# Optimization experiments

Hardware: AMD Instinct MI355X
Metric: run time of the kernel (lower is better)

Reference implementation:

```python
import jax, jax.numpy as jnp
import numpy as np

DIM = 512
HEADS = 8
HEAD_DIM = DIM // HEADS
SCALE = HEAD_DIM ** -0.5
EPS = 1e-5


def setup_inputs() -> dict:
    key = jax.random.key(0)
    ks = jax.random.split(key, 6)
    B, N, C = 4, 2048, DIM
    x = jax.random.normal(ks[0], (B, N, C), dtype=jnp.float32)
    w_qkv = jax.random.normal(ks[1], (C, 3 * C), dtype=jnp.float32) * (C ** -0.5)
    w_proj = jax.random.normal(ks[2], (C, C), dtype=jnp.float32) * (C ** -0.5)
    b_proj = jax.random.normal(ks[3], (C,), dtype=jnp.float32) * 0.02
    gamma = jnp.ones((C,), dtype=jnp.float32)
    beta = jnp.zeros((C,), dtype=jnp.float32)
    return {"x": x, "w_qkv": w_qkv, "w_proj": w_proj, "b_proj": b_proj,
            "gamma": gamma, "beta": beta}


def reference(x, w_qkv, w_proj, b_proj, gamma, beta):
    B, N, C = x.shape
    # LayerNorm over channel dim
    mu = jnp.mean(x, axis=-1, keepdims=True)
    var = jnp.mean(jnp.square(x - mu), axis=-1, keepdims=True)
    xn = (x - mu) * jax.lax.rsqrt(var + EPS) * gamma + beta
    # QKV projection (fp32, no bias)
    qkv = xn @ w_qkv  # [B, N, 3C]
    qkv = qkv.reshape(B, N, 3, HEADS, HEAD_DIM)
    q = jnp.transpose(qkv[:, :, 0], (0, 2, 1, 3))  # [B, H, N, D]
    k = jnp.transpose(qkv[:, :, 1], (0, 2, 1, 3))
    v = jnp.transpose(qkv[:, :, 2], (0, 2, 1, 3))
    attn = jnp.einsum('bhnd,bhmd->bhnm', q, k) * SCALE
    attn = jax.nn.softmax(attn, axis=-1)
    out = jnp.einsum('bhnm,bhmd->bhnd', attn, v)  # [B, H, N, D]
    out = jnp.transpose(out, (0, 2, 1, 3)).reshape(B, N, C)
    out = out @ w_proj + b_proj
    return x + out
```

## Files before the change

### kernel.cpp

```cpp
#include <hip/hip_runtime.h>
#include <hip/hip_bf16.h>
#include <math.h>

typedef _Float16 f16;
typedef _Float16 half8 __attribute__((ext_vector_type(8)));
typedef _Float16 half4 __attribute__((ext_vector_type(4)));
typedef float f32x4 __attribute__((ext_vector_type(4)));

#define DIMC 512
#define HEADS 8
#define HD 64
#define BB 4
#define NN 2048
#define MM (BB*NN)
#define NQKV (3*DIMC)
#define SCALE 0.125f
#define LOG2E 1.44269504f
#define EPSLN 1e-5f

__device__ __forceinline__ void g2l16(const void* g, void* l) {
    __builtin_amdgcn_global_load_lds(
        (const __attribute__((address_space(1))) unsigned int*)g,
        (__attribute__((address_space(3))) unsigned int*)l, 16, 0, 0);
}

__device__ __forceinline__ void ln_rows(const float* __restrict__ x,
                                        const float* __restrict__ gamma,
                                        const float* __restrict__ beta,
                                        f16* __restrict__ xn, int blk) {
    int w = threadIdx.x >> 6;
    int lane = threadIdx.x & 63;
    int row = blk * 4 + w;
    const float* xr = x + (size_t)row * DIMC;
    float4 v0 = ((const float4*)xr)[lane * 2];
    float4 v1 = ((const float4*)xr)[lane * 2 + 1];
    float s = v0.x + v0.y + v0.z + v0.w + v1.x + v1.y + v1.z + v1.w;
#pragma unroll
    for (int off = 1; off < 64; off <<= 1) s += __shfl_xor(s, off);
    float mu = s * (1.0f / DIMC);
    float d0 = v0.x - mu, d1 = v0.y - mu, d2 = v0.z - mu, d3 = v0.w - mu;
    float d4 = v1.x - mu, d5 = v1.y - mu, d6 = v1.z - mu, d7 = v1.w - mu;
    float s2 = d0*d0 + d1*d1 + d2*d2 + d3*d3 + d4*d4 + d5*d5 + d6*d6 + d7*d7;
#pragma unroll
    for (int off = 1; off < 64; off <<= 1) s2 += __shfl_xor(s2, off);
    float rstd = rsqrtf(s2 * (1.0f / DIMC) + EPSLN);
    float4 g0 = ((const float4*)gamma)[lane * 2];
    float4 g1 = ((const float4*)gamma)[lane * 2 + 1];
    float4 b0 = ((const float4*)beta)[lane * 2];
    float4 b1 = ((const float4*)beta)[lane * 2 + 1];
    half8 o;
    o[0] = (f16)(d0 * rstd * g0.x + b0.x);
    o[1] = (f16)(d1 * rstd * g0.y + b0.y);
    o[2] = (f16)(d2 * rstd * g0.z + b0.z);
    o[3] = (f16)(d3 * rstd * g0.w + b0.w);
    o[4] = (f16)(d4 * rstd * g1.x + b1.x);
    o[5] = (f16)(d5 * rstd * g1.y + b1.y);
    o[6] = (f16)(d6 * rstd * g1.z + b1.z);
    o[7] = (f16)(d7 * rstd * g1.w + b1.w);
    ((half8*)(xn + (size_t)row * DIMC))[lane] = o;
}

__device__ __forceinline__ void transp_tile(const float* __restrict__ src,
                                            f16* __restrict__ dst,
                                            int R, int C, int k0, int n0) {
    __shared__ f16 t[32][72];
    int tid = threadIdx.x;
    int rr = tid >> 6, col = tid & 63;
#pragma unroll
    for (int p = 0; p < 8; p++) {
        int r = p * 4 + rr;
        t[r][col] = (f16)src[(size_t)(k0 + r) * C + n0 + col];
    }
    __syncthreads();
    int nl = tid >> 2, kc = (tid & 3) * 8;
    half8 v;
#pragma unroll
    for (int j = 0; j < 8; j++) v[j] = t[kc + j][nl];
    *(half8*)&dst[(size_t)(n0 + nl) * R + k0 + kc] = v;
}

__global__ __launch_bounds__(256) void prep_kernel(const float* __restrict__ x,
                                                   const float* __restrict__ gamma,
                                                   const float* __restrict__ beta,
                                                   const float* __restrict__ wqkv,
                                                   const float* __restrict__ wproj,
                                                   f16* __restrict__ xn,
                                                   f16* __restrict__ wqkvt,
                                                   f16* __restrict__ wprojt) {
    int bid = blockIdx.x;
    if (bid < 2048) {
        ln_rows(x, gamma, beta, xn, bid);
    } else if (bid < 2048 + 384) {
        int b2 = bid - 2048;
        int bx = b2 % 24, by = b2 / 24;
        transp_tile(wqkv, wqkvt, DIMC, NQKV, by * 32, bx * 64);
    } else {
        int b2 = bid - 2048 - 384;
        int bx = b2 % 8, by = b2 / 8;
        transp_tile(wproj, wprojt, DIMC, DIMC, by * 32, bx * 64);
    }
}

__device__ __forceinline__ void gemm128_loop(const char* Ag, const char* Bg,
                                             f16* As, f16* Bs, f32x4 (&acc)[4][4]) {
    int tid = threadIdx.x;
    int w = tid >> 6, lane = tid & 63, l15 = lane & 15, quad = lane >> 4;
    int wy = w >> 1, wx = w & 1;
    int off0 = w * 1024 + lane * 16;
    for (int kk = 0; kk < 16; ++kk) {
        __syncthreads();
#pragma unroll
        for (int c = 0; c < 2; ++c) {
            int off = c * 4096 + off0;
            int row = off >> 6, col = off & 63;
            g2l16(Ag + (size_t)row * 1024 + kk * 64 + col, (char*)As + c * 4096 + w * 1024);
            g2l16(Bg + (size_t)row * 1024 + kk * 64 + col, (char*)Bs + c * 4096 + w * 1024);
        }
        __syncthreads();
        half8 af[4], bf[4];
#pragma unroll
        for (int i = 0; i < 4; ++i) {
            af[i] = *(const half8*)((const char*)As + ((wy * 64 + i * 16 + l15) << 6) + quad * 16);
            bf[i] = *(const half8*)((const char*)Bs + ((wx * 64 + i * 16 + l15) << 6) + quad * 16);
        }
#pragma unroll
        for (int i = 0; i < 4; ++i)
#pragma unroll
            for (int j = 0; j < 4; ++j)
                acc[i][j] = __builtin_amdgcn_mfma_f32_16x16x32_f16(af[i], bf[j], acc[i][j], 0, 0, 0);
    }
}

__global__ __launch_bounds__(256) void gemm_qkv(const f16* __restrict__ xn,
                                                const f16* __restrict__ wt,
                                                f16* __restrict__ qb,
                                                f16* __restrict__ kbuf,
                                                f16* __restrict__ vtb) {
    __shared__ __align__(16) f16 As[128 * 32];
    __shared__ __align__(16) f16 Bs[128 * 32];
    int tid = threadIdx.x;
    int w = tid >> 6, lane = tid & 63, l15 = lane & 15, quad = lane >> 4;
    int wy = w >> 1, wx = w & 1;
    int m0 = blockIdx.y * 128, c0 = blockIdx.x * 128;
    f32x4 acc[4][4] = {};
    gemm128_loop((const char*)(xn + (size_t)m0 * DIMC),
                 (const char*)(wt + (size_t)c0 * DIMC), As, Bs, acc);
    int bx = blockIdx.x;
    if (bx < 8) {
        const float QS = SCALE * LOG2E;
        f16* dst = (bx < 4) ? qb : kbuf;
        float mul = (bx < 4) ? QS : 1.0f;
        int cb = (bx < 4) ? c0 : c0 - DIMC;
#pragma unroll
        for (int i = 0; i < 4; ++i)
#pragma unroll
            for (int j = 0; j < 4; ++j)
#pragma unroll
                for (int r = 0; r < 4; ++r) {
                    int m = m0 + wy * 64 + i * 16 + quad * 4 + r;
                    int c = cb + wx * 64 + j * 16 + l15;
                    int b = m >> 11, n = m & 2047;
                    int h = c >> 6, d = c & 63;
                    dst[(((size_t)(b * HEADS + h)) * NN + n) * HD + d] = (f16)(acc[i][j][r] * mul);
                }
    } else {
        __syncthreads();
        f16* T = (f16*)As + w * 512;
        int cb = c0 - 2 * DIMC;
        int dl = lane >> 2, mp = lane & 3;
#pragma unroll
        for (int i = 0; i < 4; ++i)
#pragma unroll
            for (int j = 0; j < 4; ++j) {
                half4 hv;
#pragma unroll
                for (int r = 0; r < 4; ++r) hv[r] = (f16)acc[i][j][r];
                *(half4*)&T[l15 * 20 + quad * 4] = hv;
                half4 rv = *(half4*)&T[dl * 20 + mp * 4];
                int c = cb + wx * 64 + j * 16 + dl;
                int m = m0 + wy * 64 + i * 16 + mp * 4;
                int b = m >> 11, n = m & 2047;
                int h = c >> 6, d = c & 63;
                *(half4*)&vtb[(((size_t)(b * HEADS + h)) * HD + d) * NN + n] = rv;
            }
    }
}

__global__ __launch_bounds__(128, 4) void attn_kernel(const f16* __restrict__ qb,
                                                      const f16* __restrict__ kbuf,
                                                      const f16* __restrict__ vtb,
                                                      f16* __restrict__ ao) {
    __shared__ __align__(16) f16 KV[9216];
    f16* Ks = KV;
    f16* Vs = KV + 4608;
    int id = blockIdx.x;
    int xcd = id & 7, slot = id >> 3;
    int bh = xcd * 4 + (slot >> 5);
    int qt5 = slot & 31;
    int n0 = qt5 * 64;
    int tid = threadIdx.x, w = tid >> 6, lane = tid & 63, l15 = lane & 15, quad = lane >> 4;
    const f16* Kbase = kbuf + (size_t)bh * NN * HD;
    const f16* Vbase = vtb + (size_t)bh * HD * NN;
    const f16* Qbase = qb + (size_t)bh * NN * HD;
    half8 qf[2][2];
#pragma unroll
    for (int qt = 0; qt < 2; ++qt) {
        const f16* qr = Qbase + (size_t)(n0 + w * 32 + qt * 16 + l15) * HD + quad * 8;
        qf[qt][0] = *(const half8*)qr;
        qf[qt][1] = *(const half8*)(qr + 32);
    }
    f32x4 ot[2][4] = {};
    f32x4 lacc[2] = {};
    half4 ones;
#pragma unroll
    for (int j = 0; j < 4; ++j) ones[j] = (f16)1.0f;
    int srow = tid >> 1, part = (tid & 1) * 32;
    half8 kp[4], vp[4];
    {
        const f16* kg = Kbase + (size_t)srow * HD + part;
        const f16* vg = Vbase + (size_t)srow * NN + part;
#pragma unroll
        for (int j = 0; j < 4; ++j) {
            kp[j] = ((const half8*)kg)[j];
            vp[j] = ((const half8*)vg)[j];
        }
    }
    for (int it = 0; it < NN / 64; ++it) {
        __syncthreads();
#pragma unroll
        for (int j = 0; j < 4; ++j) {
            *(half8*)&Ks[srow * 72 + part + j * 8] = kp[j];
            *(half8*)&Vs[srow * 72 + part + j * 8] = vp[j];
        }
        __syncthreads();
        if (it < NN / 64 - 1) {
            int kt0 = (it + 1) * 64;
            const f16* kg = Kbase + (size_t)(kt0 + srow) * HD + part;
            const f16* vg = Vbase + (size_t)srow * NN + kt0 + part;
#pragma unroll
            for (int j = 0; j < 4; ++j) {
                kp[j] = ((const half8*)kg)[j];
                vp[j] = ((const half8*)vg)[j];
            }
        }
        f32x4 s0[4], s1[4];
#pragma unroll
        for (int kt = 0; kt < 4; ++kt) {
            half8 a0 = *(const half8*)&Ks[(kt * 16 + l15) * 72 + quad * 8];
            half8 a1 = *(const half8*)&Ks[(kt * 16 + l15) * 72 + 32 + quad * 8];
            f32x4 z0 = {};
            z0 = __builtin_amdgcn_mfma_f32_16x16x32_f16(a0, qf[0][0], z0, 0, 0, 0);
            z0 = __builtin_amdgcn_mfma_f32_16x16x32_f16(a1, qf[0][1], z0, 0, 0, 0);
            s0[kt] = z0;
            f32x4 z1 = {};
            z1 = __builtin_amdgcn_mfma_f32_16x16x32_f16(a0, qf[1][0], z1, 0, 0, 0);
            z1 = __builtin_amdgcn_mfma_f32_16x16x32_f16(a1, qf[1][1], z1, 0, 0, 0);
            s1[kt] = z1;
        }
        half4 pb[2][4];
#pragma unroll
        for (int kt = 0; kt < 4; ++kt) {
            half4 p0, p1;
#pragma unroll
            for (int r = 0; r < 4; ++r) {
                p0[r] = (f16)__builtin_amdgcn_exp2f(s0[kt][r]);
                p1[r] = (f16)__builtin_amdgcn_exp2f(s1[kt][r]);
            }
            pb[0][kt] = p0;
            pb[1][kt] = p1;
        }
#pragma unroll
        for (int kt = 0; kt < 4; ++kt) {
            lacc[0] = __builtin_amdgcn_mfma_f32_16x16x16f16(ones, pb[0][kt], lacc[0], 0, 0, 0);
            lacc[1] = __builtin_amdgcn_mfma_f32_16x16x16f16(ones, pb[1][kt], lacc[1], 0, 0, 0);
#pragma unroll
            for (int dt = 0; dt < 4; ++dt) {
                half4 av = *(const half4*)&Vs[(dt * 16 + l15) * 72 + kt * 16 + quad * 4];
                ot[0][dt] = __builtin_amdgcn_mfma_f32_16x16x16f16(av, pb[0][kt], ot[0][dt], 0, 0, 0);
                ot[1][dt] = __builtin_amdgcn_mfma_f32_16x16x16f16(av, pb[1][kt], ot[1][dt], 0, 0, 0);
            }
        }
    }
#pragma unroll
    for (int qt = 0; qt < 2; ++qt) {
        float inv = 1.0f / lacc[qt][0];
#pragma unroll
        for (int dt = 0; dt < 4; ++dt)
#pragma unroll
            for (int r = 0; r < 4; ++r) ot[qt][dt][r] *= inv;
    }
    __syncthreads();
    f16* T = KV + w * 2304;
#pragma unroll
    for (int qt = 0; qt < 2; ++qt)
#pragma unroll
        for (int dt = 0; dt < 4; ++dt) {
            half4 hv;
#pragma unroll
            for (int r = 0; r < 4; ++r) hv[r] = (f16)ot[qt][dt][r];
            *(half4*)&T[(qt * 16 + l15) * 72 + dt * 16 + quad * 4] = hv;
        }
    __syncthreads();
    int h = bh & 7, b = bh >> 3;
#pragma unroll
    for (int j = 0; j < 4; ++j) {
        int nl = j * 8 + (lane >> 3);
        int d8 = (lane & 7) * 8;
        half8 v = *(const half8*)&T[nl * 72 + d8];
        *(half8*)&ao[((size_t)(b * NN + n0 + w * 32 + nl)) * DIMC + h * HD + d8] = v;
    }
}

__global__ __launch_bounds__(256) void gemm_proj(const f16* __restrict__ aob,
                                                 const f16* __restrict__ wt,
                                                 const float* __restrict__ x,
                                                 const float* __restrict__ bias,
                                                 float* __restrict__ out) {
    __shared__ __align__(16) f16 As[128 * 32];
    __shared__ __align__(16) f16 Bs[64 * 32];
    int tid = threadIdx.x;
    int w = tid >> 6, lane = tid & 63, l15 = lane & 15, quad = lane >> 4;
    int m0 = blockIdx.y * 128, c0 = blockIdx.x * 64;
    const char* Ag = (const char*)(aob + (size_t)m0 * DIMC);
    const char* Bg = (const char*)(wt + (size_t)c0 * DIMC);
    f32x4 acc[2][4] = {};
    int off0 = w * 1024 + lane * 16;
    for (int kk = 0; kk < 16; ++kk) {
        __syncthreads();
#pragma unroll
        for (int c = 0; c < 2; ++c) {
            int off = c * 4096 + off0;
            int row = off >> 6, col = off & 63;
            g2l16(Ag + (size_t)row * 1024 + kk * 64 + col, (char*)As + c * 4096 + w * 1024);
        }
        {
            int off = tid * 16;
            int row = off >> 6, col = off & 63;
            g2l16(Bg + (size_t)row * 1024 + kk * 64 + col, (char*)Bs + w * 1024);
        }
        __syncthreads();
        half8 af[2], bf[4];
#pragma unroll
        for (int i = 0; i < 2; ++i)
            af[i] = *(const half8*)((const char*)As + ((w * 32 + i * 16 + l15) << 6) + quad * 16);
#pragma unroll
        for (int j = 0; j < 4; ++j)
            bf[j] = *(const half8*)((const char*)Bs + ((j * 16 + l15) << 6) + quad * 16);
#pragma unroll
        for (int i = 0; i < 2; ++i)
#pragma unroll
            for (int j = 0; j < 4; ++j)
                acc[i][j] = __builtin_amdgcn_mfma_f32_16x16x32_f16(af[i], bf[j], acc[i][j], 0, 0, 0);
    }
#pragma unroll
    for (int i = 0; i < 2; ++i)
#pragma unroll
        for (int j = 0; j < 4; ++j)
#pragma unroll
            for (int r = 0; r < 4; ++r) {
                int m = m0 + w * 32 + i * 16 + quad * 4 + r;
                int c = c0 + j * 16 + l15;
                out[(size_t)m * DIMC + c] = x[(size_t)m * DIMC + c] + bias[c] + acc[i][j][r];
            }
}

extern "C" void kernel_launch(void* const* d_in, const int* in_sizes, int n_in,
                              void* d_out, int out_size, void* d_ws, size_t ws_size,
                              hipStream_t stream) {
    (void)in_sizes; (void)n_in; (void)out_size; (void)ws_size;
    const float* x     = (const float*)d_in[0];
    const float* wqkv  = (const float*)d_in[1];
    const float* wproj = (const float*)d_in[2];
    const float* bproj = (const float*)d_in[3];
    const float* gamma = (const float*)d_in[4];
    const float* beta  = (const float*)d_in[5];
    float* out = (float*)d_out;

    char* ws = (char*)d_ws;
    f16* xn     = (f16*)ws;                 ws += (size_t)MM * DIMC * 2;
    f16* wqkvt  = (f16*)ws;                 ws += (size_t)NQKV * DIMC * 2;
    f16* wprojt = (f16*)ws;                 ws += (size_t)DIMC * DIMC * 2;
    f16* qbuf   = (f16*)ws;                 ws += (size_t)MM * DIMC * 2;
    f16* kbuf   = (f16*)ws;                 ws += (size_t)MM * DIMC * 2;
    f16* vtbuf  = (f16*)ws;                 ws += (size_t)MM * DIMC * 2;
    f16* aobuf  = (f16*)ws;                 ws += (size_t)MM * DIMC * 2;

    prep_kernel<<<2048 + 384 + 128, 256, 0, stream>>>(x, gamma, beta, wqkv, wproj,
                                                      xn, wqkvt, wprojt);
    gemm_qkv<<<dim3(NQKV / 128, MM / 128), 256, 0, stream>>>(xn, wqkvt, qbuf, kbuf, vtbuf);
    attn_kernel<<<1024, 128, 0, stream>>>(qbuf, kbuf, vtbuf, aobuf);
    gemm_proj<<<dim3(DIMC / 64, MM / 128), 256, 0, stream>>>(aobuf, wprojt, x, bproj, out);
}
```

Before: 169.3 us.

## Split attention key range across two wave groups and merge partial results

The attention block grows from 2 to 4 waves. Two groups each process half of the key/value sequence for the same 64 query rows, using separate LDS tiles, so each block finishes in half as many iterations. Group 1 then writes its fp32 partial outputs and row sums to LDS, and group 0 adds them in, normalizes and stores. This raises per-block parallelism and latency hiding at the cost of double LDS use, an extra reduction pass, and possibly lower occupancy. Merging without rescaling is valid only because the softmax here subtracts no running max.

```diff
diff --git a/kernel.cpp b/kernel.cpp
--- a/kernel.cpp
+++ b/kernel.cpp
@@ -6,6 +6,7 @@
 typedef _Float16 half8 __attribute__((ext_vector_type(8)));
 typedef _Float16 half4 __attribute__((ext_vector_type(4)));
 typedef float f32x4 __attribute__((ext_vector_type(4)));
+typedef float float4v __attribute__((ext_vector_type(4)));
 
 #define DIMC 512
 #define HEADS 8
@@ -186,26 +187,27 @@
     }
 }
 
-__global__ __launch_bounds__(128, 4) void attn_kernel(const f16* __restrict__ qb,
+__global__ __launch_bounds__(256, 4) void attn_kernel(const f16* __restrict__ qb,
                                                       const f16* __restrict__ kbuf,
                                                       const f16* __restrict__ vtb,
                                                       f16* __restrict__ ao) {
-    __shared__ __align__(16) f16 KV[9216];
-    f16* Ks = KV;
-    f16* Vs = KV + 4608;
+    __shared__ __align__(16) f16 KV[18432];
     int id = blockIdx.x;
     int xcd = id & 7, slot = id >> 3;
     int bh = xcd * 4 + (slot >> 5);
     int qt5 = slot & 31;
     int n0 = qt5 * 64;
     int tid = threadIdx.x, w = tid >> 6, lane = tid & 63, l15 = lane & 15, quad = lane >> 4;
+    int wq = w & 1, grp = w >> 1;
     const f16* Kbase = kbuf + (size_t)bh * NN * HD;
     const f16* Vbase = vtb + (size_t)bh * HD * NN;
     const f16* Qbase = qb + (size_t)bh * NN * HD;
+    f16* Ksw = KV + grp * 4608;
+    f16* Vsw = KV + 9216 + grp * 4608;
     half8 qf[2][2];
 #pragma unroll
     for (int qt = 0; qt < 2; ++qt) {
-        const f16* qr = Qbase + (size_t)(n0 + w * 32 + qt * 16 + l15) * HD + quad * 8;
+        const f16* qr = Qbase + (size_t)(n0 + wq * 32 + qt * 16 + l15) * HD + quad * 8;
         qf[qt][0] = *(const half8*)qr;
         qf[qt][1] = *(const half8*)(qr + 32);
     }
@@ -214,27 +216,32 @@
     half4 ones;
 #pragma unroll
     for (int j = 0; j < 4; ++j) ones[j] = (f16)1.0f;
-    int srow = tid >> 1, part = (tid & 1) * 32;
+    int grpS = tid >> 7;
+    int r2 = tid & 127;
+    int srow = r2 >> 1, part = (r2 & 1) * 32;
+    f16* KsS = KV + grpS * 4608;
+    f16* VsS = KV + 9216 + grpS * 4608;
+    int kbegS = grpS * 1024;
     half8 kp[4], vp[4];
     {
-        const f16* kg = Kbase + (size_t)srow * HD + part;
-        const f16* vg = Vbase + (size_t)srow * NN + part;
+        const f16* kg = Kbase + (size_t)(kbegS + srow) * HD + part;
+        const f16* vg = Vbase + (size_t)srow * NN + kbegS + part;
 #pragma unroll
         for (int j = 0; j < 4; ++j) {
             kp[j] = ((const half8*)kg)[j];
             vp[j] = ((const half8*)vg)[j];
         }
     }
-    for (int it = 0; it < NN / 64; ++it) {
+    for (int it = 0; it < 16; ++it) {
         __syncthreads();
 #pragma unroll
         for (int j = 0; j < 4; ++j) {
-            *(half8*)&Ks[srow * 72 + part + j * 8] = kp[j];
-            *(half8*)&Vs[srow * 72 + part + j * 8] = vp[j];
-        }
-        __syncthreads();
-        if (it < NN / 64 - 1) {
-            int kt0 = (it + 1) * 64;
+            *(half8*)&KsS[srow * 72 + part + j * 8] = kp[j];
+            *(half8*)&VsS[srow * 72 + part + j * 8] = vp[j];
+        }
+        __syncthreads();
+        if (it < 15) {
+            int kt0 = kbegS + (it + 1) * 64;
             const f16* kg = Kbase + (size_t)(kt0 + srow) * HD + part;
             const f16* vg = Vbase + (size_t)srow * NN + kt0 + part;
 #pragma unroll
@@ -246,8 +253,8 @@
         f32x4 s0[4], s1[4];
 #pragma unroll
         for (int kt = 0; kt < 4; ++kt) {
-            half8 a0 = *(const half8*)&Ks[(kt * 16 + l15) * 72 + quad * 8];
-            half8 a1 = *(const half8*)&Ks[(kt * 16 + l15) * 72 + 32 + quad * 8];
+            half8 a0 = *(const half8*)&Ksw[(kt * 16 + l15) * 72 + quad * 8];
+            half8 a1 = *(const half8*)&Ksw[(kt * 16 + l15) * 72 + 32 + quad * 8];
             f32x4 z0 = {};
             z0 = __builtin_amdgcn_mfma_f32_16x16x32_f16(a0, qf[0][0], z0, 0, 0, 0);
             z0 = __builtin_amdgcn_mfma_f32_16x16x32_f16(a1, qf[0][1], z0, 0, 0, 0);
@@ -275,39 +282,55 @@
             lacc[1] = __builtin_amdgcn_mfma_f32_16x16x16f16(ones, pb[1][kt], lacc[1], 0, 0, 0);
 #pragma unroll
             for (int dt = 0; dt < 4; ++dt) {
-                half4 av = *(const half4*)&Vs[(dt * 16 + l15) * 72 + kt * 16 + quad * 4];
+                half4 av = *(const half4*)&Vsw[(dt * 16 + l15) * 72 + kt * 16 + quad * 4];
                 ot[0][dt] = __builtin_amdgcn_mfma_f32_16x16x16f16(av, pb[0][kt], ot[0][dt], 0, 0, 0);
                 ot[1][dt] = __builtin_amdgcn_mfma_f32_16x16x16f16(av, pb[1][kt], ot[1][dt], 0, 0, 0);
             }
         }
     }
-#pragma unroll
-    for (int qt = 0; qt < 2; ++qt) {
-        float inv = 1.0f / lacc[qt][0];
-#pragma unroll
-        for (int dt = 0; dt < 4; ++dt)
-#pragma unroll
-            for (int r = 0; r < 4; ++r) ot[qt][dt][r] *= inv;
-    }
     __syncthreads();
-    f16* T = KV + w * 2304;
-#pragma unroll
-    for (int qt = 0; qt < 2; ++qt)
-#pragma unroll
-        for (int dt = 0; dt < 4; ++dt) {
-            half4 hv;
-#pragma unroll
-            for (int r = 0; r < 4; ++r) hv[r] = (f16)ot[qt][dt][r];
-            *(half4*)&T[(qt * 16 + l15) * 72 + dt * 16 + quad * 4] = hv;
-        }
+    float* Obuf = (float*)KV;
+    float* Lbuf = (float*)(KV + 8704);
+    if (grp == 1) {
+#pragma unroll
+        for (int qt = 0; qt < 2; ++qt) {
+#pragma unroll
+            for (int dt = 0; dt < 4; ++dt)
+                *(float4v*)&Obuf[(((wq * 2 + qt) * 4 + dt) << 8) + lane * 4] = ot[qt][dt];
+            Lbuf[(wq * 2 + qt) * 64 + lane] = lacc[qt][0];
+        }
+    }
     __syncthreads();
-    int h = bh & 7, b = bh >> 3;
-#pragma unroll
-    for (int j = 0; j < 4; ++j) {
-        int nl = j * 8 + (lane >> 3);
-        int d8 = (lane & 7) * 8;
-        half8 v = *(const half8*)&T[nl * 72 + d8];
-        *(half8*)&ao[((size_t)(b * NN + n0 + w * 32 + nl)) * DIMC + h * HD + d8] = v;
+    if (grp == 0) {
+#pragma unroll
+        for (int qt = 0; qt < 2; ++qt) {
+            float l2 = Lbuf[(wq * 2 + qt) * 64 + lane];
+            float inv = 1.0f / (lacc[qt][0] + l2);
+#pragma unroll
+            for (int dt = 0; dt < 4; ++dt) {
+                float4v o2 = *(const float4v*)&Obuf[(((wq * 2 + qt) * 4 + dt) << 8) + lane * 4];
+#pragma unroll
+                for (int r = 0; r < 4; ++r) ot[qt][dt][r] = (ot[qt][dt][r] + o2[r]) * inv;
+            }
+        }
+        f16* T = KV + 10240 + wq * 2304;
+#pragma unroll
+        for (int qt = 0; qt < 2; ++qt)
+#pragma unroll
+            for (int dt = 0; dt < 4; ++dt) {
+                half4 hv;
+#pragma unroll
+                for (int r = 0; r < 4; ++r) hv[r] = (f16)ot[qt][dt][r];
+                *(half4*)&T[(qt * 16 + l15) * 72 + dt * 16 + quad * 4] = hv;
+            }
+        int h = bh & 7, b = bh >> 3;
+#pragma unroll
+        for (int j = 0; j < 4; ++j) {
+            int nl = j * 8 + (lane >> 3);
+            int d8 = (lane & 7) * 8;
+            half8 v = *(const half8*)&T[nl * 72 + d8];
+            *(half8*)&ao[((size_t)(b * NN + n0 + wq * 32 + nl)) * DIMC + h * HD + d8] = v;
+        }
     }
 }
 
@@ -388,6 +411,6 @@
     prep_kernel<<<2048 + 384 + 128, 256, 0, stream>>>(x, gamma, beta, wqkv, wproj,
                                                       xn, wqkvt, wprojt);
     gemm_qkv<<<dim3(NQKV / 128, MM / 128), 256, 0, stream>>>(xn, wqkvt, qbuf, kbuf, vtbuf);
-    attn_kernel<<<1024, 128, 0, stream>>>(qbuf, kbuf, vtbuf, aobuf);
+    attn_kernel<<<1024, 256, 0, stream>>>(qbuf, kbuf, vtbuf, aobuf);
     gemm_proj<<<dim3(DIMC / 64, MM / 128), 256, 0, stream>>>(aobuf, wprojt, x, bproj, out);
 }
```

Measured after the change: 168.3 us. No clear change (-0.6%).
